# Kernel tuning notes

Hardware: AMD Instinct MI355X
Metric: run time of the kernel (lower is better)

## Reference

```python
import math
import jax, jax.numpy as jnp
import numpy as np

B, K_LEN, Q_LEN = 16, 1024, 1024
E, N_HEAD, H = 1024, 8, 128

def setup_inputs() -> dict:
    key = jax.random.key(0)
    ks = jax.random.split(key, 7)
    k = jax.random.normal(ks[0], (B, K_LEN, E), dtype=jnp.float32)
    q = jax.random.normal(ks[1], (B, Q_LEN, E), dtype=jnp.float32)
    w_kx = jax.random.normal(ks[2], (N_HEAD, E, H), dtype=jnp.float32) * (1.0 / math.sqrt(E))
    w_qx = jax.random.normal(ks[3], (N_HEAD, E, H), dtype=jnp.float32) * (1.0 / math.sqrt(E))
    proj_w = jax.random.normal(ks[4], (E, N_HEAD * H), dtype=jnp.float32) * (1.0 / math.sqrt(N_HEAD * H))
    proj_b = jax.random.normal(ks[5], (E,), dtype=jnp.float32) * 0.01
    memory_len = jax.random.randint(ks[6], (B,), 0, K_LEN, dtype=jnp.int32)
    return {"k": k, "q": q, "w_kx": w_kx, "w_qx": w_qx, "proj_w": proj_w, "proj_b": proj_b, "memory_len": memory_len}

def reference(k, q, w_kx, w_qx, proj_w, proj_b, memory_len):
    n_head, embed_dim, hidden = w_kx.shape
    mb, k_len, _ = k.shape
    q_len = q.shape[1]
    # Faithful replication of torch repeat/view pairing:
    # row idx in [0, n_head*mb): data batch = idx % mb, weight head = idx % n_head
    idx = jnp.arange(n_head * mb)
    kx = jnp.einsum('nse,neh->nsh', k[idx % mb], w_kx[idx % n_head])   # [nB, k_len, H]
    qx = jnp.einsum('nse,neh->nsh', q[idx % mb], w_qx[idx % n_head])   # [nB, q_len, H]
    score = jnp.einsum('nqh,nkh->nqk', qx, kx) / math.sqrt(hidden)     # [nB, q_len, k_len]
    # 1D memory_len path: per-batch key-length mask, tiled over heads
    valid = jnp.arange(k_len)[None, :] < memory_len[:, None]           # [B, k_len]
    valid = jnp.tile(valid, (n_head, 1))[:, None, :]                   # [nB, 1, k_len]
    score = jnp.where(valid, score, jnp.float32(-10000.0))
    attn = jax.nn.softmax(score, axis=-1)
    out = jnp.einsum('nqk,nkh->nqh', attn, kx)                         # [nB, q_len, H]
    # torch.cat(torch.split(out, mb, 0), -1): chunk j -> feature block j
    out = out.reshape(n_head, mb, q_len, hidden).transpose(1, 2, 0, 3).reshape(mb, q_len, n_head * hidden)
    out = out @ proj_w.T + proj_b                                      # [B, q_len, E]
    return out, attn
```

## Files before the change

kernel.cpp:

```cpp
#include <hip/hip_runtime.h>
#include <hip/hip_bf16.h>

#define NBATCH 16
#define SEQ    1024
#define EDIM   1024
#define HDIM   128
#define RSQRT_H 0.08838834764831845f


typedef short s8b  __attribute__((ext_vector_type(8)));
typedef float f32x4 __attribute__((ext_vector_type(4)));
typedef float f4v  __attribute__((ext_vector_type(4)));

__device__ __forceinline__ unsigned short bfr(float f) {
    unsigned u = __float_as_uint(f);
    u += 0x7fffu + ((u >> 16) & 1u);
    return (unsigned short)(u >> 16);
}

__device__ __forceinline__ f32x4 MFMA(s8b a, s8b b, f32x4 c) {
    return __builtin_amdgcn_mfma_f32_16x16x32_bf16(a, b, c, 0, 0, 0);
}

__device__ __forceinline__ void quad_transpose(int d, const float y[4], float z[4]) {
    float s0 = (d & 1) ? y[0] : y[1];
    float g0 = __shfl_xor(s0, 1);
    float s1 = (d & 1) ? y[2] : y[3];
    float g1 = __shfl_xor(s1, 1);
    float B0 = (d & 1) ? g0 : y[0];
    float B1 = (d & 1) ? y[1] : g0;
    float B2 = (d & 1) ? g1 : y[2];
    float B3 = (d & 1) ? y[3] : g1;
    float s2 = (d & 2) ? B0 : B2;
    float h0 = __shfl_xor(s2, 2);
    float s3 = (d & 2) ? B1 : B3;
    float h1 = __shfl_xor(s3, 2);
    z[0] = (d & 2) ? h0 : B0;
    z[1] = (d & 2) ? h1 : B1;
    z[2] = (d & 2) ? B2 : h0;
    z[3] = (d & 2) ? B3 : h1;
}

__global__ __launch_bounds__(256) void projx_mfma(const float* __restrict__ X,
                                                  const unsigned short* __restrict__ WT,
                                                  unsigned short* __restrict__ OUT) {
    const int b  = blockIdx.y;
    const int bm = blockIdx.x * 32;
    const int lane = threadIdx.x & 63, w = threadIdx.x >> 6;
    const int wn = w * 32;
    const int r = lane & 15, ko4 = lane >> 4, ko = ko4 * 8;

    const unsigned short* Bb = WT + (size_t)(b & 7) * 131072 + (size_t)(wn + r) * 1024 + ko;
    const float* Ab = X + (size_t)b * 1048576 + (size_t)(bm + r) * 1024 + ko;
    f32x4 acc[2][2] = {};

    for (int k = 0; k < 1024; k += 32) {
        s8b a0, a1;
        float4 u0 = *(const float4*)(Ab + k);
        float4 u1 = *(const float4*)(Ab + k + 4);
        a0[0]=(short)bfr(u0.x); a0[1]=(short)bfr(u0.y);
        a0[2]=(short)bfr(u0.z); a0[3]=(short)bfr(u0.w);
        a0[4]=(short)bfr(u1.x); a0[5]=(short)bfr(u1.y);
        a0[6]=(short)bfr(u1.z); a0[7]=(short)bfr(u1.w);
        float4 v0 = *(const float4*)(Ab + (size_t)16 * 1024 + k);
        float4 v1 = *(const float4*)(Ab + (size_t)16 * 1024 + k + 4);
        a1[0]=(short)bfr(v0.x); a1[1]=(short)bfr(v0.y);
        a1[2]=(short)bfr(v0.z); a1[3]=(short)bfr(v0.w);
        a1[4]=(short)bfr(v1.x); a1[5]=(short)bfr(v1.y);
        a1[6]=(short)bfr(v1.z); a1[7]=(short)bfr(v1.w);
        s8b b0 = *(const s8b*)(Bb + k);
        s8b b1 = *(const s8b*)(Bb + (size_t)16 * 1024 + k);
        acc[0][0] = MFMA(a0, b0, acc[0][0]);
        acc[0][1] = MFMA(a0, b1, acc[0][1]);
        acc[1][0] = MFMA(a1, b0, acc[1][0]);
        acc[1][1] = MFMA(a1, b1, acc[1][1]);
    }
#pragma unroll
    for (int i = 0; i < 2; ++i)
#pragma unroll
    for (int j = 0; j < 2; ++j) {
        const int row0 = bm + i * 16 + ko4 * 4;
        const int col  = wn + j * 16 + r;
#pragma unroll
        for (int jj = 0; jj < 4; ++jj)
            OUT[((size_t)b * SEQ + row0 + jj) * HDIM + col] = bfr(acc[i][j][jj]);
    }
}

__global__ __launch_bounds__(256) void weff_kernel(const float* __restrict__ proj_w,
                                                   unsigned short* __restrict__ weffb) {
    int i = blockIdx.x * 256 + threadIdx.x;
    int e = i >> 7, h = i & 127;
    const float* p = proj_w + (size_t)e * (8 * HDIM) + h;
    float s = 0.f;
#pragma unroll
    for (int j = 0; j < 8; ++j) s += p[j * HDIM];
    weffb[i] = bfr(s);
}

__global__ __launch_bounds__(256) void wt_kernel(const float* __restrict__ src,
                                                 unsigned short* __restrict__ dst) {
    __shared__ unsigned short tile[32][40];
    const int hd = blockIdx.z, e0 = blockIdx.x * 32, h0 = blockIdx.y * 32;
    const int t = threadIdx.x, r = t >> 3, c = (t & 7) * 4;
    float4 v = *(const float4*)(src + ((size_t)hd * 1024 + e0 + r) * 128 + h0 + c);
    tile[r][c]     = bfr(v.x);
    tile[r][c + 1] = bfr(v.y);
    tile[r][c + 2] = bfr(v.z);
    tile[r][c + 3] = bfr(v.w);
    __syncthreads();
    ushort4 o;
    o.x = tile[c][r]; o.y = tile[c + 1][r]; o.z = tile[c + 2][r]; o.w = tile[c + 3][r];
    *(ushort4*)(dst + ((size_t)hd * 128 + h0 + r) * 1024 + e0 + c) = o;
}

__global__ __launch_bounds__(256) void kxt_kernel(const unsigned short* __restrict__ src,
                                                  unsigned short* __restrict__ dst) {
    __shared__ unsigned short tile[32][40];
    const int b = blockIdx.z, s0 = blockIdx.x * 32, h0 = blockIdx.y * 32;
    const int t = threadIdx.x, r = t >> 3, c = (t & 7) * 4;
    *(ushort4*)&tile[r][c] =
        *(const ushort4*)(src + ((size_t)b * 1024 + s0 + r) * 128 + h0 + c);
    __syncthreads();
    ushort4 o;
    o.x = tile[c][r]; o.y = tile[c + 1][r]; o.z = tile[c + 2][r]; o.w = tile[c + 3][r];
    *(ushort4*)(dst + ((size_t)b * 128 + h0 + r) * 1024 + s0 + c) = o;
}

__global__ __launch_bounds__(256) void fused_attn(
        const unsigned short* __restrict__ qxh, const unsigned short* __restrict__ kxh,
        const unsigned short* __restrict__ kxT, const unsigned short* __restrict__ weffb,
        const float* __restrict__ proj_b, const int* __restrict__ mlen,
        float* __restrict__ attn0, float* __restrict__ out0, int wr_all) {
    __shared__ unsigned short Ph[16][1048];
    __shared__ unsigned short PVa[16][132];
    __shared__ float redm[4][16];
    __shared__ float redl[4][16];

    const int flat = blockIdx.y * 64 + blockIdx.x;
    const int work = (flat & 7) * 128 + (flat >> 3);
    const int b  = work >> 6;
    const int q0 = (work & 63) * 16;

    const int t = threadIdx.x, w = t >> 6, lane = t & 63;
    const int r = lane & 15, ko4 = lane >> 4, ko = ko4 * 8;
    const int d = r & 3;
    const int cb = r & 12;
    const int trow = ko4 * 4 + d;
    const int ml = mlen[b];

    s8b aq[4];
#pragma unroll
    for (int ks = 0; ks < 4; ++ks)
        aq[ks] = *(const s8b*)(qxh + ((size_t)b * SEQ + q0 + r) * HDIM + ks * 32 + ko);

    f32x4 sacc[16];
#pragma unroll
    for (int i = 0; i < 16; ++i) {
        const int n0 = (w + 4 * i) * 16;
        f32x4 acc = {};
#pragma unroll
        for (int ks = 0; ks < 4; ++ks) {
            s8b bk = *(const s8b*)(kxh + ((size_t)b * SEQ + n0 + r) * HDIM + ks * 32 + ko);
            acc = MFMA(aq[ks], bk, acc);
        }
        sacc[i] = acc;
    }

    float pm[4] = {-3.0e38f, -3.0e38f, -3.0e38f, -3.0e38f};
#pragma unroll
    for (int i = 0; i < 16; ++i) {
        const int col = (w + 4 * i) * 16 + r;
#pragma unroll
        for (int jj = 0; jj < 4; ++jj) {
            float x = sacc[i][jj] * RSQRT_H;
            x = (col < ml) ? x : -10000.0f;
            sacc[i][jj] = x;
            pm[jj] = fmaxf(pm[jj], x);
        }
    }
#pragma unroll
    for (int dd = 1; dd < 16; dd <<= 1)
#pragma unroll
        for (int jj = 0; jj < 4; ++jj) pm[jj] = fmaxf(pm[jj], __shfl_xor(pm[jj], dd));
    if (r == 0) {
#pragma unroll
        for (int jj = 0; jj < 4; ++jj) redm[w][ko4 * 4 + jj] = pm[jj];
    }
    __syncthreads();
    float m[4];
#pragma unroll
    for (int jj = 0; jj < 4; ++jj) {
        const int row = ko4 * 4 + jj;
        m[jj] = fmaxf(fmaxf(redm[0][row], redm[1][row]),
                      fmaxf(redm[2][row], redm[3][row]));
    }
    float pl[4] = {0.f, 0.f, 0.f, 0.f};
#pragma unroll
    for (int i = 0; i < 16; ++i)
#pragma unroll
        for (int jj = 0; jj < 4; ++jj) {
            float e = __expf(sacc[i][jj] - m[jj]);
            sacc[i][jj] = e;
            pl[jj] += e;
        }
#pragma unroll
    for (int dd = 1; dd < 16; dd <<= 1)
#pragma unroll
        for (int jj = 0; jj < 4; ++jj) pl[jj] += __shfl_xor(pl[jj], dd);
    if (r == 0) {
#pragma unroll
        for (int jj = 0; jj < 4; ++jj) redl[w][ko4 * 4 + jj] = pl[jj];
    }
    __syncthreads();
    float li[4];
#pragma unroll
    for (int jj = 0; jj < 4; ++jj) {
        const int row = ko4 * 4 + jj;
        li[jj] = 1.0f / (redl[0][row] + redl[1][row] + redl[2][row] + redl[3][row]);
    }

    const size_t RB = (size_t)NBATCH * SEQ * SEQ;
    float* base0 = attn0 + (size_t)b * SEQ * SEQ + (size_t)(q0 + trow) * SEQ;
    const bool wr2 = wr_all || (b >= 5);
#pragma unroll
    for (int i = 0; i < 16; ++i) {
        const int n0 = (w + 4 * i) * 16;
        float y[4], z[4];
#pragma unroll
        for (int jj = 0; jj < 4; ++jj) y[jj] = sacc[i][jj] * li[jj];
        quad_transpose(d, y, z);
        f4v y4 = {z[0], z[1], z[2], z[3]};
        float* p0 = base0 + n0 + cb;
        *(f4v*)(p0)          = y4;
        *(f4v*)(p0 + RB)     = y4;
        *(f4v*)(p0 + 3 * RB) = y4;
        *(f4v*)(p0 + 4 * RB) = y4;
        *(f4v*)(p0 + 5 * RB) = y4;
        *(f4v*)(p0 + 6 * RB) = y4;
        *(f4v*)(p0 + 7 * RB) = y4;
        if (wr2) *(f4v*)(p0 + 2 * RB) = y4;
        uint2 pk;
        pk.x = (unsigned)bfr(z[0]) | ((unsigned)bfr(z[1]) << 16);
        pk.y = (unsigned)bfr(z[2]) | ((unsigned)bfr(z[3]) << 16);
        *(uint2*)(&Ph[trow][n0 + cb]) = pk;
    }
    __syncthreads();

    f32x4 acc2[2] = {};
    for (int ks = 0; ks < 32; ++ks) {
        s8b pa = *(const s8b*)(&Ph[r][ks * 32 + ko]);
#pragma unroll
        for (int c = 0; c < 2; ++c) {
            const int n0 = (w * 2 + c) * 16;
            s8b bk = *(const s8b*)(kxT + ((size_t)b * HDIM + n0 + r) * SEQ + ks * 32 + ko);
            acc2[c] = MFMA(pa, bk, acc2[c]);
        }
    }
#pragma unroll
    for (int c = 0; c < 2; ++c) {
        const int n0 = (w * 2 + c) * 16;
#pragma unroll
        for (int jj = 0; jj < 4; ++jj)
            PVa[ko4 * 4 + jj][n0 + r] = bfr(acc2[c][jj]);
    }
    __syncthreads();

    s8b av[4];
#pragma unroll
    for (int ks = 0; ks < 4; ++ks)
        av[ks] = *(const s8b*)(&PVa[r][ks * 32 + ko]);
    float* ob = out0 + (size_t)b * SEQ * EDIM + (size_t)(q0 + trow) * EDIM;
#pragma unroll
    for (int i = 0; i < 16; ++i) {
        const int e0 = (w + 4 * i) * 16;
        f32x4 acc = {};
#pragma unroll
        for (int ks = 0; ks < 4; ++ks) {
            s8b bk = *(const s8b*)(weffb + (size_t)(e0 + r) * HDIM + ks * 32 + ko);
            acc = MFMA(av[ks], bk, acc);
        }
        float y[4] = {acc[0], acc[1], acc[2], acc[3]}, z[4];
        quad_transpose(d, y, z);
        f4v bias4 = *(const f4v*)(proj_b + e0 + cb);
        f4v o4 = {z[0] + bias4.x, z[1] + bias4.y, z[2] + bias4.z, z[3] + bias4.w};
        *(f4v*)(ob + e0 + cb) = o4;
    }
}

__global__ __launch_bounds__(256) void fixup_kernel(const uint4* __restrict__ src,
                                                    uint4* __restrict__ dst) {
    size_t i = (size_t)blockIdx.x * 256 + threadIdx.x;
    dst[i] = src[i];
}

extern "C" void kernel_launch(void* const* d_in, const int* in_sizes, int n_in,
                              void* d_out, int out_size, void* d_ws, size_t ws_size,
                              hipStream_t stream) {
    const float* k      = (const float*)d_in[0];
    const float* q      = (const float*)d_in[1];
    const float* w_kx   = (const float*)d_in[2];
    const float* w_qx   = (const float*)d_in[3];
    const float* proj_w = (const float*)d_in[4];
    const float* proj_b = (const float*)d_in[5];
    const int*   mlen   = (const int*)d_in[6];

    float* out0  = (float*)d_out;
    float* attn0 = out0 + (size_t)NBATCH * SEQ * EDIM;
    const size_t BLK = (size_t)NBATCH * SEQ * SEQ;

    const size_t SCRATCH_SHORTS = 1048576ull * 2 + 131072 + 2097152ull * 3;
    const size_t NEED = SCRATCH_SHORTS * 2;
    const int use_ws = (ws_size >= NEED) ? 1 : 0;

    unsigned short* sc16 = use_ws ? (unsigned short*)d_ws
                                  : (unsigned short*)(attn0 + 2 * BLK);
    unsigned short* wkT   = sc16;
    unsigned short* wqT   = wkT + 1048576;
    unsigned short* weffb = wqT + 1048576;
    unsigned short* qxh   = weffb + 131072;
    unsigned short* kxh   = qxh + 2097152;
    unsigned short* kxT   = kxh + 2097152;

    weff_kernel<<<512, 256, 0, stream>>>(proj_w, weffb);
    wt_kernel<<<dim3(32, 4, 8), 256, 0, stream>>>(w_kx, wkT);
    wt_kernel<<<dim3(32, 4, 8), 256, 0, stream>>>(w_qx, wqT);

    projx_mfma<<<dim3(32, 16), 256, 0, stream>>>(k, wkT, kxh);
    projx_mfma<<<dim3(32, 16), 256, 0, stream>>>(q, wqT, qxh);

    kxt_kernel<<<dim3(32, 4, 16), 256, 0, stream>>>(kxh, kxT);

    fused_attn<<<dim3(64, 16), 256, 0, stream>>>(qxh, kxh, kxT, weffb, proj_b,
                                                 mlen, attn0, out0, use_ws);

    if (!use_ws)
        fixup_kernel<<<5120, 256, 0, stream>>>((const uint4*)attn0,
                                               (uint4*)(attn0 + 2 * BLK));
}
```

Measured before the change: 303.4 us.

## Merge prep kernels, combine K/Q projections, emit transposed K from projection

Folds the weight-transpose and weight-sum kernels into a single prep launch, and runs the K and Q projections in one grid of twice the size. The K projection also writes its transposed bf16 copy directly from registers, so the separate kxt transpose kernel is gone. This cuts launches from six to two and removes one pass that re-read kx from memory. In exchange the transposed store is a scattered 8-byte write per lane, and the prep kernel carries branch divergence between block types.

```diff
diff --git a/kernel.cpp b/kernel.cpp
--- a/kernel.cpp
+++ b/kernel.cpp
@@ -41,14 +41,59 @@
     z[3] = (d & 2) ? B3 : h1;
 }
 
-__global__ __launch_bounds__(256) void projx_mfma(const float* __restrict__ X,
-                                                  const unsigned short* __restrict__ WT,
-                                                  unsigned short* __restrict__ OUT) {
-    const int b  = blockIdx.y;
+__global__ __launch_bounds__(256) void prep_kernel(const float* __restrict__ w_kx,
+                                                   const float* __restrict__ w_qx,
+                                                   const float* __restrict__ proj_w,
+                                                   unsigned short* __restrict__ wkT,
+                                                   unsigned short* __restrict__ wqT,
+                                                   unsigned short* __restrict__ weffb) {
+    __shared__ unsigned short tile[32][40];
+    const int blk = blockIdx.x;
+    const int t = threadIdx.x;
+    if (blk < 2048) {
+        const int idx = blk & 1023;
+        const float* src = (blk < 1024) ? w_kx : w_qx;
+        unsigned short* dst = (blk < 1024) ? wkT : wqT;
+        const int e0 = (idx & 31) * 32, h0 = ((idx >> 5) & 3) * 32, hd = idx >> 7;
+        const int r = t >> 3, c = (t & 7) * 4;
+        float4 v = *(const float4*)(src + ((size_t)hd * 1024 + e0 + r) * 128 + h0 + c);
+        tile[r][c]     = bfr(v.x);
+        tile[r][c + 1] = bfr(v.y);
+        tile[r][c + 2] = bfr(v.z);
+        tile[r][c + 3] = bfr(v.w);
+        __syncthreads();
+        ushort4 o;
+        o.x = tile[c][r]; o.y = tile[c + 1][r]; o.z = tile[c + 2][r]; o.w = tile[c + 3][r];
+        *(ushort4*)(dst + ((size_t)hd * 128 + h0 + r) * 1024 + e0 + c) = o;
+    } else {
+        int i = (blk - 2048) * 256 + t;
+        int e = i >> 7, h = i & 127;
+        const float* p = proj_w + (size_t)e * (8 * HDIM) + h;
+        float s = 0.f;
+#pragma unroll
+        for (int j = 0; j < 8; ++j) s += p[j * HDIM];
+        weffb[i] = bfr(s);
+    }
+}
+
+__global__ __launch_bounds__(256) void projx_mfma(const float* __restrict__ K,
+                                                  const float* __restrict__ Q,
+                                                  const unsigned short* __restrict__ wkT,
+                                                  const unsigned short* __restrict__ wqT,
+                                                  unsigned short* __restrict__ kxh,
+                                                  unsigned short* __restrict__ qxh,
+                                                  unsigned short* __restrict__ kxT) {
+    const int by = blockIdx.y;
+    const bool isK = by < 16;
+    const int b  = by & 15;
     const int bm = blockIdx.x * 32;
     const int lane = threadIdx.x & 63, w = threadIdx.x >> 6;
     const int wn = w * 32;
     const int r = lane & 15, ko4 = lane >> 4, ko = ko4 * 8;
+
+    const float* X = isK ? K : Q;
+    const unsigned short* WT = isK ? wkT : wqT;
+    unsigned short* OUT = isK ? kxh : qxh;
 
     const unsigned short* Bb = WT + (size_t)(b & 7) * 131072 + (size_t)(wn + r) * 1024 + ko;
     const float* Ab = X + (size_t)b * 1048576 + (size_t)(bm + r) * 1024 + ko;
@@ -81,50 +126,21 @@
     for (int j = 0; j < 2; ++j) {
         const int row0 = bm + i * 16 + ko4 * 4;
         const int col  = wn + j * 16 + r;
-#pragma unroll
-        for (int jj = 0; jj < 4; ++jj)
-            OUT[((size_t)b * SEQ + row0 + jj) * HDIM + col] = bfr(acc[i][j][jj]);
-    }
-}
-
-__global__ __launch_bounds__(256) void weff_kernel(const float* __restrict__ proj_w,
-                                                   unsigned short* __restrict__ weffb) {
-    int i = blockIdx.x * 256 + threadIdx.x;
-    int e = i >> 7, h = i & 127;
-    const float* p = proj_w + (size_t)e * (8 * HDIM) + h;
-    float s = 0.f;
-#pragma unroll
-    for (int j = 0; j < 8; ++j) s += p[j * HDIM];
-    weffb[i] = bfr(s);
-}
-
-__global__ __launch_bounds__(256) void wt_kernel(const float* __restrict__ src,
-                                                 unsigned short* __restrict__ dst) {
-    __shared__ unsigned short tile[32][40];
-    const int hd = blockIdx.z, e0 = blockIdx.x * 32, h0 = blockIdx.y * 32;
-    const int t = threadIdx.x, r = t >> 3, c = (t & 7) * 4;
-    float4 v = *(const float4*)(src + ((size_t)hd * 1024 + e0 + r) * 128 + h0 + c);
-    tile[r][c]     = bfr(v.x);
-    tile[r][c + 1] = bfr(v.y);
-    tile[r][c + 2] = bfr(v.z);
-    tile[r][c + 3] = bfr(v.w);
-    __syncthreads();
-    ushort4 o;
-    o.x = tile[c][r]; o.y = tile[c + 1][r]; o.z = tile[c + 2][r]; o.w = tile[c + 3][r];
-    *(ushort4*)(dst + ((size_t)hd * 128 + h0 + r) * 1024 + e0 + c) = o;
-}
-
-__global__ __launch_bounds__(256) void kxt_kernel(const unsigned short* __restrict__ src,
-                                                  unsigned short* __restrict__ dst) {
-    __shared__ unsigned short tile[32][40];
-    const int b = blockIdx.z, s0 = blockIdx.x * 32, h0 = blockIdx.y * 32;
-    const int t = threadIdx.x, r = t >> 3, c = (t & 7) * 4;
-    *(ushort4*)&tile[r][c] =
-        *(const ushort4*)(src + ((size_t)b * 1024 + s0 + r) * 128 + h0 + c);
-    __syncthreads();
-    ushort4 o;
-    o.x = tile[c][r]; o.y = tile[c + 1][r]; o.z = tile[c + 2][r]; o.w = tile[c + 3][r];
-    *(ushort4*)(dst + ((size_t)b * 128 + h0 + r) * 1024 + s0 + c) = o;
+        unsigned short h0 = bfr(acc[i][j][0]);
+        unsigned short h1 = bfr(acc[i][j][1]);
+        unsigned short h2 = bfr(acc[i][j][2]);
+        unsigned short h3 = bfr(acc[i][j][3]);
+        OUT[((size_t)b * SEQ + row0 + 0) * HDIM + col] = h0;
+        OUT[((size_t)b * SEQ + row0 + 1) * HDIM + col] = h1;
+        OUT[((size_t)b * SEQ + row0 + 2) * HDIM + col] = h2;
+        OUT[((size_t)b * SEQ + row0 + 3) * HDIM + col] = h3;
+        if (isK) {
+            uint2 pk;
+            pk.x = (unsigned)h0 | ((unsigned)h1 << 16);
+            pk.y = (unsigned)h2 | ((unsigned)h3 << 16);
+            *(uint2*)(kxT + ((size_t)b * HDIM + col) * SEQ + row0) = pk;
+        }
+    }
 }
 
 __global__ __launch_bounds__(256) void fused_attn(
@@ -322,14 +338,9 @@
     unsigned short* kxh   = qxh + 2097152;
     unsigned short* kxT   = kxh + 2097152;
 
-    weff_kernel<<<512, 256, 0, stream>>>(proj_w, weffb);
-    wt_kernel<<<dim3(32, 4, 8), 256, 0, stream>>>(w_kx, wkT);
-    wt_kernel<<<dim3(32, 4, 8), 256, 0, stream>>>(w_qx, wqT);
-
-    projx_mfma<<<dim3(32, 16), 256, 0, stream>>>(k, wkT, kxh);
-    projx_mfma<<<dim3(32, 16), 256, 0, stream>>>(q, wqT, qxh);
-
-    kxt_kernel<<<dim3(32, 4, 16), 256, 0, stream>>>(kxh, kxT);
+    prep_kernel<<<2560, 256, 0, stream>>>(w_kx, w_qx, proj_w, wkT, wqT, weffb);
+
+    projx_mfma<<<dim3(32, 32), 256, 0, stream>>>(k, q, wkT, wqT, kxh, qxh, kxT);
 
     fused_attn<<<dim3(64, 16), 256, 0, stream>>>(qxh, kxh, kxT, weffb, proj_b,
                                                  mlen, attn0, out0, use_ws);
```

Result: slower. 309.6 us (+2.0%).
